# Performance work log

Hardware: AMD Instinct MI355X
Metric: run time of the kernel (lower is better)

The kernel has to match this reference:

```python
import jax, jax.numpy as jnp
import numpy as np

EPS = 1e-5
K = 3          # num adjacency subsets
V = 25         # joints
C_IN = 64
C_OUT = 128


def setup_inputs() -> dict:
    key = jax.random.key(0)
    ks = jax.random.split(key, 10)
    x = jax.random.normal(ks[0], (64, C_IN, 128, V), dtype=jnp.float32)
    # learnable adjacency (K, V, V)
    A = jax.random.normal(ks[1], (K, V, V), dtype=jnp.float32) * 0.1
    # main 1x1 conv: C_in -> C_out*K
    Wc = jax.random.normal(ks[2], (C_OUT * K, C_IN), dtype=jnp.float32) * (1.0 / np.sqrt(C_IN))
    bc = jax.random.normal(ks[3], (C_OUT * K,), dtype=jnp.float32) * 0.01
    # BN affine params (training mode -> batch stats)
    gamma = jnp.ones((C_OUT,), dtype=jnp.float32)
    beta = jnp.zeros((C_OUT,), dtype=jnp.float32)
    # residual downsample: conv1x1 C_in->C_out + BN
    Wd = jax.random.normal(ks[4], (C_OUT, C_IN), dtype=jnp.float32) * (1.0 / np.sqrt(C_IN))
    bd = jax.random.normal(ks[5], (C_OUT,), dtype=jnp.float32) * 0.01
    gamma_d = jnp.ones((C_OUT,), dtype=jnp.float32)
    beta_d = jnp.zeros((C_OUT,), dtype=jnp.float32)
    return {"x": x, "A": A, "Wc": Wc, "bc": bc, "gamma": gamma, "beta": beta,
            "Wd": Wd, "bd": bd, "gamma_d": gamma_d, "beta_d": beta_d}


def _batchnorm2d(y, gamma, beta):
    # training-mode BN over (N, T, V) per channel; biased variance like torch
    mean = jnp.mean(y, axis=(0, 2, 3), keepdims=True)
    var = jnp.var(y, axis=(0, 2, 3), keepdims=True)
    inv = jax.lax.rsqrt(var + EPS)
    return (y - mean) * inv * gamma[None, :, None, None] + beta[None, :, None, None]


def reference(x, A, Wc, bc, gamma, beta, Wd, bd, gamma_d, beta_d):
    N, C, T, Vv = x.shape
    # residual path: 1x1 conv + BN
    res = jnp.einsum('nctv,oc->notv', x, Wd) + bd[None, :, None, None]
    res = _batchnorm2d(res, gamma_d, beta_d)
    # main path: 1x1 conv -> (N, K, C_out, T, V)
    y = jnp.einsum('nctv,oc->notv', x, Wc) + bc[None, :, None, None]
    y = y.reshape(N, K, C_OUT, T, Vv)
    # graph aggregation over K subsets
    y = jnp.einsum('nkctv,kvw->nctw', y, A)
    y = _batchnorm2d(y, gamma, beta)
    return jax.nn.relu(y + res)
```

## Files before the change

### kernel.cpp

```cpp
#include <hip/hip_runtime.h>
#include <hip/hip_bf16.h>

typedef __attribute__((ext_vector_type(8)))  short short8;
typedef __attribute__((ext_vector_type(4)))  float floatx4;
typedef __attribute__((ext_vector_type(16))) float floatx16;

#define N_   64
#define CIN  64
#define T_   128
#define V_   25
#define CO   128
#define MCNT 204800.0f

#define OFF_WCF  0
#define OFF_WDF  98304
#define OFF_AF   131072
#define OFF_CBD  137216
#define OFF_P1   153600
#define OFF_SUM  4347904
#define OFF_STAT 4349952

__device__ __forceinline__ ushort f2bf(float f) {
    uint u = __float_as_uint(f);
    return (ushort)((u + 0x7FFFu + ((u >> 16) & 1u)) >> 16);
}
__device__ __forceinline__ uint pack2(float a, float b) {
    return (uint)f2bf(a) | ((uint)f2bf(b) << 16);
}
__device__ __forceinline__ uint pk2(float a, float b) {
    __hip_bfloat162 h = __float22bfloat162_rn(make_float2(a, b));
    union { __hip_bfloat162 h2; uint u; } cv; cv.h2 = h;
    return cv.u;
}

__global__ void k0_prep(const float* __restrict__ A, const float* __restrict__ Wc,
                        const float* __restrict__ bc, const float* __restrict__ Wd,
                        const float* __restrict__ bd, void* __restrict__ wsv) {
    char* wsb = (char*)wsv;
    ushort* WCF = (ushort*)(wsb + OFF_WCF);
    ushort* WDF = (ushort*)(wsb + OFF_WDF);
    ushort* AFp = (ushort*)(wsb + OFF_AF);
    uint*   CBD = (uint*)(wsb + OFF_CBD);
    int tid = blockIdx.x * 256 + threadIdx.x;
    int stride = gridDim.x * 256;
    for (int e = tid; e < 24576; e += stride) {
        int fe = e >> 3, el = e & 7;
        int l = fe & 63, q = fe >> 6;
        int ct = q / 12, ks = q % 12;
        int j = ks*16 + ((l >> 5) << 3) + el;
        int c = ct*32 + (l & 31);
        int k = j >> 6, ci = j & 63;
        WCF[e] = f2bf(Wc[(k * CO + c) * CIN + ci]);
    }
    for (int e = tid; e < 8192; e += stride) {
        int fe = e >> 3, el = e & 7;
        int l = fe & 63, q = fe >> 6;
        int ct = q >> 2, ks = q & 3;
        int ci = ks*16 + ((l >> 5) << 3) + el;
        int c = ct*32 + (l & 31);
        WDF[e] = f2bf(Wd[c * CIN + ci]);
    }
    for (int e = tid; e < 3072; e += stride) {
        int fe = e >> 3, el = e & 7;
        int l = fe & 63, q = fe >> 6;
        int k = q >> 1, nt = q & 1;
        int w = nt*16 + (l & 15);
        int v = (l >> 4)*8 + el;
        AFp[e] = (v < V_ && w < V_) ? f2bf(A[(k*V_ + v)*V_ + w]) : (ushort)0;
    }
    for (int e = tid; e < 4096; e += stride) {
        int c = e >> 5, w = e & 31;
        float s = 0.f;
        if (w < V_) {
            for (int k = 0; k < 3; ++k) {
                float cs = 0.f;
                for (int v = 0; v < V_; ++v) cs += A[(k*V_ + v)*V_ + w];
                s += bc[k*CO + c] * cs;
            }
        }
        CBD[e] = pack2(s, bd[c]);
    }
}

__global__ __launch_bounds__(512, 4) void k1_main(
        const float* __restrict__ x, void* __restrict__ wsv, uint* __restrict__ outu) {
    char* wsb = (char*)wsv;
    const ushort* WCF = (const ushort*)(wsb + OFF_WCF);
    const ushort* WDF = (const ushort*)(wsb + OFF_WDF);
    const ushort* AF  = (const ushort*)(wsb + OFF_AF);
    const uint*   CBD = (const uint*)(wsb + OFF_CBD);
    float* P1 = (float*)(wsb + OFF_P1);

    __shared__ uint SM[14336];
    ushort* XR   = (ushort*)SM;
    short8* XR8  = (short8*)SM;
    uint*   XRu  = SM;
    uint*   BBu0 = SM + 4096;
    uint*   BBu1 = SM + 8192;
    short8* BB8_0 = (short8*)BBu0;
    short8* BB8_1 = (short8*)BBu1;
    uint*   OST  = SM;

    const int tid = threadIdx.x;
    const int l = tid & 63, wv = tid >> 6;
    const int blk = blockIdx.x;
    const int nb = blk >> 5;
    const int r_ = blk & 31;
    const int tcb = (r_ & 7)*4 + (r_ >> 3);
    const long xbase = (long)nb * (CIN * T_ * V_);
    const int tg0 = tcb * 4;
    const int ct = wv >> 1, nh = wv & 1;
    const int h = l >> 5, w32 = l & 31;
    const int t_a = wv & 3, nt_a = wv >> 2;

    #pragma unroll
    for (int i = 0; i < 8; ++i) {
        int p = tid + i * 512;
        int ci = p >> 6, rem = p & 63, t = rem >> 4, vp = rem & 15, v = vp * 2;
        float f0 = 0.f, f1 = 0.f;
        if (v < V_)     f0 = x[xbase + ci*(T_*V_) + (tg0 + t)*V_ + v];
        if (v + 1 < V_) f1 = x[xbase + ci*(T_*V_) + (tg0 + t)*V_ + v + 1];
        int idx = (ci*4 + t)*16 + 4*((v >> 3) ^ (ci & 3)) + ((v & 7) >> 1);
        XRu[idx] = pk2(f0, f1);
    }
    __syncthreads();

    short8 xf[4];
    #pragma unroll
    for (int mt = 0; mt < 4; ++mt) {
        int ci = mt*16 + (l & 15), vg = l >> 4;
        xf[mt] = XR8[(ci*4 + t_a)*4 + (vg ^ (ci & 3))];
    }
    short8 amv[3];
    #pragma unroll
    for (int k = 0; k < 3; ++k)
        amv[k] = *(const short8*)(AF + ((k*2 + nt_a)*64 + l)*8);

    floatx16 acc0, acc1;
    #pragma unroll
    for (int i = 0; i < 16; ++i) { acc0[i] = 0.f; acc1[i] = 0.f; }

    const int g = l >> 4;
    for (int k = 0; k < 3; ++k) {
        uint* bw = (k & 1) ? BBu1 : BBu0;
        const short8* br = (k & 1) ? BB8_1 : BB8_0;
        #pragma unroll
        for (int mt = 0; mt < 4; ++mt) {
            floatx4 agc = __builtin_amdgcn_mfma_f32_16x16x32_bf16(
                xf[mt], amv[k], (floatx4){0,0,0,0}, 0, 0, 0);
            uint u0 = pk2(agc[0], agc[1]);
            uint u1 = pk2(agc[2], agc[3]);
            int l_tgt = nt_a*16 + (l & 15) + 32*(g >> 1);
            int byteoff = ((mt*4 + t_a)*64 + l_tgt)*16 + (g & 1)*8;
            uint2 tmp; tmp.x = u0; tmp.y = u1;
            *(uint2*)((char*)bw + byteoff) = tmp;
        }
        __syncthreads();
        #pragma unroll
        for (int s = 0; s < 4; ++s) {
            short8 a = *(const short8*)(WCF + ((ct*12 + k*4 + s)*64 + l)*8);
            acc0 = __builtin_amdgcn_mfma_f32_32x32x16_bf16(
                a, br[(s*4 + nh*2 + 0)*64 + l], acc0, 0, 0, 0);
            acc1 = __builtin_amdgcn_mfma_f32_32x32x16_bf16(
                a, br[(s*4 + nh*2 + 1)*64 + l], acc1, 0, 0, 0);
        }
    }

    uint cbdv[16];
    #pragma unroll
    for (int r = 0; r < 16; ++r) {
        int c = ct*32 + (r & 3) + 4*h + 8*(r >> 2);
        cbdv[r] = CBD[c*32 + w32];
    }

    #pragma unroll
    for (int i = 0; i < 2; ++i) {
        int task = tid + i*512;
        int fid = task >> 6, le = task & 63;
        int ks = fid >> 2, nt = fid & 3;
        int wq = le & 31, hh = le >> 5;
        int cib = ks*16 + hh*8;
        short8 r8;
        #pragma unroll
        for (int e = 0; e < 8; ++e) {
            int ci = cib + e;
            r8[e] = (short)XR[ci*128 + nt*32 + 8*((wq >> 3) ^ (e & 3)) + (wq & 7)];
        }
        BB8_1[fid*64 + le] = r8;
    }
    __syncthreads();

    floatx16 racc0, racc1;
    #pragma unroll
    for (int i = 0; i < 16; ++i) { racc0[i] = 0.f; racc1[i] = 0.f; }
    #pragma unroll
    for (int s = 0; s < 4; ++s) {
        short8 a = *(const short8*)(WDF + ((ct*4 + s)*64 + l)*8);
        racc0 = __builtin_amdgcn_mfma_f32_32x32x16_bf16(
            a, BB8_1[(s*4 + nh*2 + 0)*64 + l], racc0, 0, 0, 0);
        racc1 = __builtin_amdgcn_mfma_f32_32x32x16_bf16(
            a, BB8_1[(s*4 + nh*2 + 1)*64 + l], racc1, 0, 0, 0);
    }
    __syncthreads();

    if (w32 < V_) {
        #pragma unroll
        for (int r = 0; r < 16; ++r) {
            int c = ct*32 + (r & 3) + 4*h + 8*(r >> 2);
            float b0 = __uint_as_float(cbdv[r] << 16);
            float d0 = __uint_as_float(cbdv[r] & 0xFFFF0000u);
            OST[c*100 + (nh*2 + 0)*25 + w32] = pk2(acc0[r] + b0, racc0[r] + d0);
            OST[c*100 + (nh*2 + 1)*25 + w32] = pk2(acc1[r] + b0, racc1[r] + d0);
        }
    }
    __syncthreads();

    const long ob = (long)nb * 409600 + (long)tg0 * 25;
    for (int task = tid; task < 3200; task += 512) {
        int c = (task * 1311) >> 15;
        int q = task - c * 25;
        uint4 v4 = *(const uint4*)(OST + c*100 + q*4);
        *(uint4*)(outu + ob + (long)c*3200 + q*4) = v4;
    }

    {
        int cS = tid >> 2, q4 = tid & 3;
        int s0 = (q4 == 0) ? 0 : 4 + q4*24;
        int n4 = (q4 == 0) ? 7 : 6;
        const uint4* op = (const uint4*)(OST + cS*100 + s0);
        float ys = 0.f, yss = 0.f, rs = 0.f, rss = 0.f;
        #pragma unroll
        for (int j = 0; j < 7; ++j) {
            if (j < n4) {
                uint4 u = op[j];
                #pragma unroll
                for (int e = 0; e < 4; ++e) {
                    uint uu = (e == 0) ? u.x : (e == 1) ? u.y : (e == 2) ? u.z : u.w;
                    float yv = __uint_as_float(uu << 16);
                    float rv = __uint_as_float(uu & 0xFFFF0000u);
                    ys += yv; yss += yv*yv; rs += rv; rss += rv*rv;
                }
            }
        }
        ys  += __shfl_xor(ys, 1);  ys  += __shfl_xor(ys, 2);
        yss += __shfl_xor(yss, 1); yss += __shfl_xor(yss, 2);
        rs  += __shfl_xor(rs, 1);  rs  += __shfl_xor(rs, 2);
        rss += __shfl_xor(rss, 1); rss += __shfl_xor(rss, 2);
        if (q4 == 0) {
            P1[(long)blk*512 + 0*128 + cS] = ys;
            P1[(long)blk*512 + 1*128 + cS] = yss;
            P1[(long)blk*512 + 2*128 + cS] = rs;
            P1[(long)blk*512 + 3*128 + cS] = rss;
        }
    }
}

__global__ void k2a(void* __restrict__ wsv) {
    char* wsb = (char*)wsv;
    const float* P1 = (const float*)(wsb + OFF_P1);
    float* SUM = (float*)(wsb + OFF_SUM);
    __shared__ float red[256];
    int gc = blockIdx.x;
    float s = 0.f;
    for (int i = threadIdx.x; i < 2048; i += 256) s += P1[(long)i*512 + gc];
    red[threadIdx.x] = s; __syncthreads();
    for (int st = 128; st > 0; st >>= 1) {
        if (threadIdx.x < st) red[threadIdx.x] += red[threadIdx.x + st];
        __syncthreads();
    }
    if (threadIdx.x == 0) SUM[gc] = red[0];
}

__global__ void k2b(const float* __restrict__ gamma, const float* __restrict__ beta,
                    const float* __restrict__ gamma_d, const float* __restrict__ beta_d,
                    void* __restrict__ wsv) {
    char* wsb = (char*)wsv;
    const float* SUM = (const float*)(wsb + OFF_SUM);
    float* STAT = (float*)(wsb + OFF_STAT);
    int c = threadIdx.x;
    if (c < 128) {
        float my = SUM[c] / MCNT;
        float vy = fmaxf(SUM[128 + c] / MCNT - my*my, 0.f);
        float s1 = rsqrtf(vy + 1e-5f) * gamma[c];
        float h1 = beta[c] - my * s1;
        float mr = SUM[256 + c] / MCNT;
        float vr = fmaxf(SUM[384 + c] / MCNT - mr*mr, 0.f);
        float s2 = rsqrtf(vr + 1e-5f) * gamma_d[c];
        float h2 = beta_d[c] - mr * s2;
        STAT[c] = s1; STAT[128 + c] = s2; STAT[256 + c] = h1 + h2;
    }
}

__global__ __launch_bounds__(256) void k3_map(void* __restrict__ wsv, uint* __restrict__ outu) {
    const float* STAT = (const float*)((const char*)wsv + OFF_STAT);
    __shared__ float sS[384];
    for (int i = threadIdx.x; i < 384; i += 256) sS[i] = STAT[i];
    __syncthreads();
    const int total4 = 6553600;
    int stride = gridDim.x * blockDim.x;
    for (int j = blockIdx.x * blockDim.x + threadIdx.x; j < total4; j += stride) {
        uint4 u = ((const uint4*)outu)[j];
        int c = (j / 800) & 127;
        float s1 = sS[c], s2 = sS[128 + c], h = sS[256 + c];
        float4 o;
        o.x = fmaxf(__uint_as_float(u.x << 16) * s1 + __uint_as_float(u.x & 0xFFFF0000u) * s2 + h, 0.f);
        o.y = fmaxf(__uint_as_float(u.y << 16) * s1 + __uint_as_float(u.y & 0xFFFF0000u) * s2 + h, 0.f);
        o.z = fmaxf(__uint_as_float(u.z << 16) * s1 + __uint_as_float(u.z & 0xFFFF0000u) * s2 + h, 0.f);
        o.w = fmaxf(__uint_as_float(u.w << 16) * s1 + __uint_as_float(u.w & 0xFFFF0000u) * s2 + h, 0.f);
        ((float4*)outu)[j] = o;
    }
}

extern "C" void kernel_launch(void* const* d_in, const int* in_sizes, int n_in,
                              void* d_out, int out_size, void* d_ws, size_t ws_size,
                              hipStream_t stream) {
    const float* x       = (const float*)d_in[0];
    const float* A       = (const float*)d_in[1];
    const float* Wc      = (const float*)d_in[2];
    const float* bc      = (const float*)d_in[3];
    const float* gamma   = (const float*)d_in[4];
    const float* beta    = (const float*)d_in[5];
    const float* Wd      = (const float*)d_in[6];
    const float* bd      = (const float*)d_in[7];
    const float* gamma_d = (const float*)d_in[8];
    const float* beta_d  = (const float*)d_in[9];
    uint* outu = (uint*)d_out;

    k0_prep<<<32, 256, 0, stream>>>(A, Wc, bc, Wd, bd, d_ws);
    k1_main<<<2048, 512, 0, stream>>>(x, d_ws, outu);
    k2a<<<512, 256, 0, stream>>>(d_ws);
    k2b<<<1, 128, 0, stream>>>(gamma, beta, gamma_d, beta_d, d_ws);
    k3_map<<<2048, 256, 0, stream>>>(d_ws, outu);
}
```

Baseline: 107.2 us.

## Make k1_main persistent over four time tiles with register-prefetched x loads

```diff
diff --git a/kernel.cpp b/kernel.cpp
--- a/kernel.cpp
+++ b/kernel.cpp
@@ -91,7 +91,7 @@
     const uint*   CBD = (const uint*)(wsb + OFF_CBD);
     float* P1 = (float*)(wsb + OFF_P1);
 
-    __shared__ uint SM[14336];
+    __shared__ uint SM[16896];
     ushort* XR   = (ushort*)SM;
     short8* XR8  = (short8*)SM;
     uint*   XRu  = SM;
@@ -99,158 +99,189 @@
     uint*   BBu1 = SM + 8192;
     short8* BB8_0 = (short8*)BBu0;
     short8* BB8_1 = (short8*)BBu1;
-    uint*   OST  = SM;
+    uint*   OST  = SM + 4096;
 
     const int tid = threadIdx.x;
     const int l = tid & 63, wv = tid >> 6;
     const int blk = blockIdx.x;
-    const int nb = blk >> 5;
-    const int r_ = blk & 31;
-    const int tcb = (r_ & 7)*4 + (r_ >> 3);
+    const int nb = blk >> 3, tg = blk & 7;
     const long xbase = (long)nb * (CIN * T_ * V_);
-    const int tg0 = tcb * 4;
     const int ct = wv >> 1, nh = wv & 1;
     const int h = l >> 5, w32 = l & 31;
     const int t_a = wv & 3, nt_a = wv >> 2;
+    const int g = l >> 4;
+
+    float sf0[8], sf1[8];
 
     #pragma unroll
     for (int i = 0; i < 8; ++i) {
         int p = tid + i * 512;
         int ci = p >> 6, rem = p & 63, t = rem >> 4, vp = rem & 15, v = vp * 2;
-        float f0 = 0.f, f1 = 0.f;
-        if (v < V_)     f0 = x[xbase + ci*(T_*V_) + (tg0 + t)*V_ + v];
-        if (v + 1 < V_) f1 = x[xbase + ci*(T_*V_) + (tg0 + t)*V_ + v + 1];
+        sf0[i] = 0.f; sf1[i] = 0.f;
+        if (v < V_)     sf0[i] = x[xbase + ci*(T_*V_) + (tg*16 + t)*V_ + v];
+        if (v + 1 < V_) sf1[i] = x[xbase + ci*(T_*V_) + (tg*16 + t)*V_ + v + 1];
+    }
+    #pragma unroll
+    for (int i = 0; i < 8; ++i) {
+        int p = tid + i * 512;
+        int ci = p >> 6, rem = p & 63, t = rem >> 4, vp = rem & 15, v = vp * 2;
         int idx = (ci*4 + t)*16 + 4*((v >> 3) ^ (ci & 3)) + ((v & 7) >> 1);
-        XRu[idx] = pk2(f0, f1);
-    }
-    __syncthreads();
-
-    short8 xf[4];
-    #pragma unroll
-    for (int mt = 0; mt < 4; ++mt) {
-        int ci = mt*16 + (l & 15), vg = l >> 4;
-        xf[mt] = XR8[(ci*4 + t_a)*4 + (vg ^ (ci & 3))];
-    }
-    short8 amv[3];
-    #pragma unroll
-    for (int k = 0; k < 3; ++k)
-        amv[k] = *(const short8*)(AF + ((k*2 + nt_a)*64 + l)*8);
-
-    floatx16 acc0, acc1;
-    #pragma unroll
-    for (int i = 0; i < 16; ++i) { acc0[i] = 0.f; acc1[i] = 0.f; }
-
-    const int g = l >> 4;
-    for (int k = 0; k < 3; ++k) {
-        uint* bw = (k & 1) ? BBu1 : BBu0;
-        const short8* br = (k & 1) ? BB8_1 : BB8_0;
+        XRu[idx] = pk2(sf0[i], sf1[i]);
+    }
+
+    for (int s = 0; s < 4; ++s) {
+        const int tcb = tg*4 + s;
+        const int tg0 = tcb * 4;
+        __syncthreads();
+
+        if (s < 3) {
+            #pragma unroll
+            for (int i = 0; i < 8; ++i) {
+                int p = tid + i * 512;
+                int ci = p >> 6, rem = p & 63, t = rem >> 4, vp = rem & 15, v = vp * 2;
+                sf0[i] = 0.f; sf1[i] = 0.f;
+                if (v < V_)     sf0[i] = x[xbase + ci*(T_*V_) + (tg0 + 4 + t)*V_ + v];
+                if (v + 1 < V_) sf1[i] = x[xbase + ci*(T_*V_) + (tg0 + 4 + t)*V_ + v + 1];
+            }
+        }
+
+        short8 xf[4];
         #pragma unroll
         for (int mt = 0; mt < 4; ++mt) {
-            floatx4 agc = __builtin_amdgcn_mfma_f32_16x16x32_bf16(
-                xf[mt], amv[k], (floatx4){0,0,0,0}, 0, 0, 0);
-            uint u0 = pk2(agc[0], agc[1]);
-            uint u1 = pk2(agc[2], agc[3]);
-            int l_tgt = nt_a*16 + (l & 15) + 32*(g >> 1);
-            int byteoff = ((mt*4 + t_a)*64 + l_tgt)*16 + (g & 1)*8;
-            uint2 tmp; tmp.x = u0; tmp.y = u1;
-            *(uint2*)((char*)bw + byteoff) = tmp;
-        }
-        __syncthreads();
-        #pragma unroll
-        for (int s = 0; s < 4; ++s) {
-            short8 a = *(const short8*)(WCF + ((ct*12 + k*4 + s)*64 + l)*8);
-            acc0 = __builtin_amdgcn_mfma_f32_32x32x16_bf16(
-                a, br[(s*4 + nh*2 + 0)*64 + l], acc0, 0, 0, 0);
-            acc1 = __builtin_amdgcn_mfma_f32_32x32x16_bf16(
-                a, br[(s*4 + nh*2 + 1)*64 + l], acc1, 0, 0, 0);
-        }
-    }
-
-    uint cbdv[16];
-    #pragma unroll
-    for (int r = 0; r < 16; ++r) {
-        int c = ct*32 + (r & 3) + 4*h + 8*(r >> 2);
-        cbdv[r] = CBD[c*32 + w32];
-    }
-
-    #pragma unroll
-    for (int i = 0; i < 2; ++i) {
-        int task = tid + i*512;
-        int fid = task >> 6, le = task & 63;
-        int ks = fid >> 2, nt = fid & 3;
-        int wq = le & 31, hh = le >> 5;
-        int cib = ks*16 + hh*8;
-        short8 r8;
-        #pragma unroll
-        for (int e = 0; e < 8; ++e) {
-            int ci = cib + e;
-            r8[e] = (short)XR[ci*128 + nt*32 + 8*((wq >> 3) ^ (e & 3)) + (wq & 7)];
-        }
-        BB8_1[fid*64 + le] = r8;
-    }
-    __syncthreads();
-
-    floatx16 racc0, racc1;
-    #pragma unroll
-    for (int i = 0; i < 16; ++i) { racc0[i] = 0.f; racc1[i] = 0.f; }
-    #pragma unroll
-    for (int s = 0; s < 4; ++s) {
-        short8 a = *(const short8*)(WDF + ((ct*4 + s)*64 + l)*8);
-        racc0 = __builtin_amdgcn_mfma_f32_32x32x16_bf16(
-            a, BB8_1[(s*4 + nh*2 + 0)*64 + l], racc0, 0, 0, 0);
-        racc1 = __builtin_amdgcn_mfma_f32_32x32x16_bf16(
-            a, BB8_1[(s*4 + nh*2 + 1)*64 + l], racc1, 0, 0, 0);
-    }
-    __syncthreads();
-
-    if (w32 < V_) {
+            int ci = mt*16 + (l & 15), vg = l >> 4;
+            xf[mt] = XR8[(ci*4 + t_a)*4 + (vg ^ (ci & 3))];
+        }
+        short8 amv[3];
+        #pragma unroll
+        for (int k = 0; k < 3; ++k)
+            amv[k] = *(const short8*)(AF + ((k*2 + nt_a)*64 + l)*8);
+
+        floatx16 acc0, acc1;
+        #pragma unroll
+        for (int i = 0; i < 16; ++i) { acc0[i] = 0.f; acc1[i] = 0.f; }
+
+        for (int k = 0; k < 3; ++k) {
+            uint* bw = (k & 1) ? BBu1 : BBu0;
+            const short8* br = (k & 1) ? BB8_1 : BB8_0;
+            #pragma unroll
+            for (int mt = 0; mt < 4; ++mt) {
+                floatx4 agc = __builtin_amdgcn_mfma_f32_16x16x32_bf16(
+                    xf[mt], amv[k], (floatx4){0,0,0,0}, 0, 0, 0);
+                uint u0 = pk2(agc[0], agc[1]);
+                uint u1 = pk2(agc[2], agc[3]);
+                int l_tgt = nt_a*16 + (l & 15) + 32*(g >> 1);
+                int byteoff = ((mt*4 + t_a)*64 + l_tgt)*16 + (g & 1)*8;
+                uint2 tmp; tmp.x = u0; tmp.y = u1;
+                *(uint2*)((char*)bw + byteoff) = tmp;
+            }
+            __syncthreads();
+            #pragma unroll
+            for (int ss = 0; ss < 4; ++ss) {
+                short8 a = *(const short8*)(WCF + ((ct*12 + k*4 + ss)*64 + l)*8);
+                acc0 = __builtin_amdgcn_mfma_f32_32x32x16_bf16(
+                    a, br[(ss*4 + nh*2 + 0)*64 + l], acc0, 0, 0, 0);
+                acc1 = __builtin_amdgcn_mfma_f32_32x32x16_bf16(
+                    a, br[(ss*4 + nh*2 + 1)*64 + l], acc1, 0, 0, 0);
+            }
+        }
+
+        uint cbdv[16];
         #pragma unroll
         for (int r = 0; r < 16; ++r) {
             int c = ct*32 + (r & 3) + 4*h + 8*(r >> 2);
-            float b0 = __uint_as_float(cbdv[r] << 16);
-            float d0 = __uint_as_float(cbdv[r] & 0xFFFF0000u);
-            OST[c*100 + (nh*2 + 0)*25 + w32] = pk2(acc0[r] + b0, racc0[r] + d0);
-            OST[c*100 + (nh*2 + 1)*25 + w32] = pk2(acc1[r] + b0, racc1[r] + d0);
-        }
-    }
-    __syncthreads();
-
-    const long ob = (long)nb * 409600 + (long)tg0 * 25;
-    for (int task = tid; task < 3200; task += 512) {
-        int c = (task * 1311) >> 15;
-        int q = task - c * 25;
-        uint4 v4 = *(const uint4*)(OST + c*100 + q*4);
-        *(uint4*)(outu + ob + (long)c*3200 + q*4) = v4;
-    }
-
-    {
-        int cS = tid >> 2, q4 = tid & 3;
-        int s0 = (q4 == 0) ? 0 : 4 + q4*24;
-        int n4 = (q4 == 0) ? 7 : 6;
-        const uint4* op = (const uint4*)(OST + cS*100 + s0);
-        float ys = 0.f, yss = 0.f, rs = 0.f, rss = 0.f;
-        #pragma unroll
-        for (int j = 0; j < 7; ++j) {
-            if (j < n4) {
-                uint4 u = op[j];
-                #pragma unroll
-                for (int e = 0; e < 4; ++e) {
-                    uint uu = (e == 0) ? u.x : (e == 1) ? u.y : (e == 2) ? u.z : u.w;
-                    float yv = __uint_as_float(uu << 16);
-                    float rv = __uint_as_float(uu & 0xFFFF0000u);
-                    ys += yv; yss += yv*yv; rs += rv; rss += rv*rv;
+            cbdv[r] = CBD[c*32 + w32];
+        }
+
+        #pragma unroll
+        for (int i = 0; i < 2; ++i) {
+            int task = tid + i*512;
+            int fid = task >> 6, le = task & 63;
+            int ks = fid >> 2, nt = fid & 3;
+            int wq = le & 31, hh = le >> 5;
+            int cib = ks*16 + hh*8;
+            short8 r8;
+            #pragma unroll
+            for (int e = 0; e < 8; ++e) {
+                int ci = cib + e;
+                r8[e] = (short)XR[ci*128 + nt*32 + 8*((wq >> 3) ^ (e & 3)) + (wq & 7)];
+            }
+            BB8_1[fid*64 + le] = r8;
+        }
+        __syncthreads();
+
+        floatx16 racc0, racc1;
+        #pragma unroll
+        for (int i = 0; i < 16; ++i) { racc0[i] = 0.f; racc1[i] = 0.f; }
+        #pragma unroll
+        for (int ss = 0; ss < 4; ++ss) {
+            short8 a = *(const short8*)(WDF + ((ct*4 + ss)*64 + l)*8);
+            racc0 = __builtin_amdgcn_mfma_f32_32x32x16_bf16(
+                a, BB8_1[(ss*4 + nh*2 + 0)*64 + l], racc0, 0, 0, 0);
+            racc1 = __builtin_amdgcn_mfma_f32_32x32x16_bf16(
+                a, BB8_1[(ss*4 + nh*2 + 1)*64 + l], racc1, 0, 0, 0);
+        }
+        __syncthreads();
+
+        if (s < 3) {
+            #pragma unroll
+            for (int i = 0; i < 8; ++i) {
+                int p = tid + i * 512;
+                int ci = p >> 6, rem = p & 63, t = rem >> 4, vp = rem & 15, v = vp * 2;
+                int idx = (ci*4 + t)*16 + 4*((v >> 3) ^ (ci & 3)) + ((v & 7) >> 1);
+                XRu[idx] = pk2(sf0[i], sf1[i]);
+            }
+        }
+
+        if (w32 < V_) {
+            #pragma unroll
+            for (int r = 0; r < 16; ++r) {
+                int c = ct*32 + (r & 3) + 4*h + 8*(r >> 2);
+                float b0 = __uint_as_float(cbdv[r] << 16);
+                float d0 = __uint_as_float(cbdv[r] & 0xFFFF0000u);
+                OST[c*100 + (nh*2 + 0)*25 + w32] = pk2(acc0[r] + b0, racc0[r] + d0);
+                OST[c*100 + (nh*2 + 1)*25 + w32] = pk2(acc1[r] + b0, racc1[r] + d0);
+            }
+        }
+        __syncthreads();
+
+        const long ob = (long)nb * 409600 + (long)tg0 * 25;
+        for (int task = tid; task < 3200; task += 512) {
+            int c = (task * 1311) >> 15;
+            int q = task - c * 25;
+            uint4 v4 = *(const uint4*)(OST + c*100 + q*4);
+            *(uint4*)(outu + ob + (long)c*3200 + q*4) = v4;
+        }
+
+        {
+            int cS = tid >> 2, q4 = tid & 3;
+            int s0 = (q4 == 0) ? 0 : 4 + q4*24;
+            int n4 = (q4 == 0) ? 7 : 6;
+            const uint4* op = (const uint4*)(OST + cS*100 + s0);
+            float ys = 0.f, yss = 0.f, rs = 0.f, rss = 0.f;
+            #pragma unroll
+            for (int j = 0; j < 7; ++j) {
+                if (j < n4) {
+                    uint4 u = op[j];
+                    #pragma unroll
+                    for (int e = 0; e < 4; ++e) {
+                        uint uu = (e == 0) ? u.x : (e == 1) ? u.y : (e == 2) ? u.z : u.w;
+                        float yv = __uint_as_float(uu << 16);
+                        float rv = __uint_as_float(uu & 0xFFFF0000u);
+                        ys += yv; yss += yv*yv; rs += rv; rss += rv*rv;
+                    }
                 }
             }
-        }
-        ys  += __shfl_xor(ys, 1);  ys  += __shfl_xor(ys, 2);
-        yss += __shfl_xor(yss, 1); yss += __shfl_xor(yss, 2);
-        rs  += __shfl_xor(rs, 1);  rs  += __shfl_xor(rs, 2);
-        rss += __shfl_xor(rss, 1); rss += __shfl_xor(rss, 2);
-        if (q4 == 0) {
-            P1[(long)blk*512 + 0*128 + cS] = ys;
-            P1[(long)blk*512 + 1*128 + cS] = yss;
-            P1[(long)blk*512 + 2*128 + cS] = rs;
-            P1[(long)blk*512 + 3*128 + cS] = rss;
+            ys  += __shfl_xor(ys, 1);  ys  += __shfl_xor(ys, 2);
+            yss += __shfl_xor(yss, 1); yss += __shfl_xor(yss, 2);
+            rs  += __shfl_xor(rs, 1);  rs  += __shfl_xor(rs, 2);
+            rss += __shfl_xor(rss, 1); rss += __shfl_xor(rss, 2);
+            if (q4 == 0) {
+                long row = (long)(blk*4 + s) * 512;
+                P1[row + 0*128 + cS] = ys;
+                P1[row + 1*128 + cS] = yss;
+                P1[row + 2*128 + cS] = rs;
+                P1[row + 3*128 + cS] = rss;
+            }
         }
     }
 }
@@ -327,7 +358,7 @@
     uint* outu = (uint*)d_out;
 
     k0_prep<<<32, 256, 0, stream>>>(A, Wc, bc, Wd, bd, d_ws);
-    k1_main<<<2048, 512, 0, stream>>>(x, d_ws, outu);
+    k1_main<<<512, 512, 0, stream>>>(x, d_ws, outu);
     k2a<<<512, 256, 0, stream>>>(d_ws);
     k2b<<<1, 128, 0, stream>>>(gamma, beta, gamma_d, beta_d, d_ws);
     k3_map<<<2048, 256, 0, stream>>>(d_ws, outu);
```

Result: slower. 301.5 us (+181.1%).
